# Kernel tuning notes

Hardware: AMD Instinct MI355X
Metric: run time of the kernel (lower is better)

Reference implementation:

```python
import jax, jax.numpy as jnp
import numpy as np

N_NODES = 50000
N_EDGES = 800000
HIDDEN = 256
OUT_DIM = 10
LN_EPS = 1e-5


def setup_inputs() -> dict:
    key = jax.random.key(0)
    ks = jax.random.split(key, 8)
    return {
        "node_features": jax.random.normal(ks[0], (N_NODES, 2), dtype=jnp.float32),
        "edge_index": jax.random.randint(ks[1], (2, N_EDGES), 0, N_NODES, dtype=jnp.int64),
        "W_gcn": jax.random.normal(ks[2], (2, HIDDEN), dtype=jnp.float32) / np.sqrt(2.0),
        "b_gcn": jnp.zeros((HIDDEN,), dtype=jnp.float32),
        "ln_gamma": jnp.ones((HIDDEN,), dtype=jnp.float32),
        "ln_beta": jnp.zeros((HIDDEN,), dtype=jnp.float32),
        "W_h": jax.random.normal(ks[3], (HIDDEN, HIDDEN), dtype=jnp.float32) / np.sqrt(HIDDEN),
        "b_h": jnp.zeros((HIDDEN,), dtype=jnp.float32),
        "W_out": jax.random.normal(ks[4], (HIDDEN, OUT_DIM), dtype=jnp.float32) / np.sqrt(HIDDEN),
        "b_out": jnp.zeros((OUT_DIM,), dtype=jnp.float32),
    }


def reference(node_features, edge_index, W_gcn, b_gcn, ln_gamma, ln_beta, W_h, b_h, W_out, b_out):
    N = node_features.shape[0]
    # --- GCNConv (PyG default): add self-loops + symmetric normalization ---
    loop = jnp.arange(N, dtype=edge_index.dtype)
    src = jnp.concatenate([edge_index[0], loop])
    dst = jnp.concatenate([edge_index[1], loop])
    deg = jax.ops.segment_sum(jnp.ones_like(dst, dtype=node_features.dtype), dst, num_segments=N)
    dinv = jnp.where(deg > 0, jax.lax.rsqrt(deg), 0.0)
    norm = dinv[src] * dinv[dst]  # [E+N]
    h = node_features @ W_gcn  # [N, H], d_in=2 so linear-before-propagate
    msgs = h[src] * norm[:, None]  # [E+N, H] gathered messages
    agg = jax.ops.segment_sum(msgs, dst, num_segments=N) + b_gcn  # scatter-add
    h = jax.nn.relu(agg)
    # --- LayerNorm ---
    mu = jnp.mean(h, axis=-1, keepdims=True)
    var = jnp.mean(jnp.square(h - mu), axis=-1, keepdims=True)
    h = (h - mu) * jax.lax.rsqrt(var + LN_EPS) * ln_gamma + ln_beta
    # --- global_add_pool with batch = zeros(N): one graph ---
    pooled = jnp.sum(h, axis=0, keepdims=True)  # [1, H]
    # --- MLP head ---
    z = jax.nn.relu(pooled @ W_h + b_h)
    logits = z @ W_out + b_out  # [1, OUT_DIM]
    return jax.nn.log_softmax(logits, axis=1)
```

## Files before the change

kernel.cpp:

```cpp
#include <hip/hip_runtime.h>
#include <math.h>

#define N_NODES 50000
#define N_EDGES 800000
#define HIDDEN  256
#define OUT_DIM 10
#define LN_EPS  1e-5f

#define NP    8
#define PART  6250
#define ES    32
#define EPSE  (N_EDGES / ES)
#define EPSE4 (EPSE / 4)
#define NH2   (N_NODES / 2)
#define NPB   64
#define LNB   ((N_NODES + NPB - 1) / NPB)

__global__ __launch_bounds__(1024) void hist_kernel(
    const int4* __restrict__ dst4, unsigned* __restrict__ degp32,
    float* __restrict__ pooled8,
    const float4* __restrict__ Wh4, const float4* __restrict__ Wo4)
{
    __shared__ unsigned hist[PART];
    const int tid = threadIdx.x;
    const int s = blockIdx.x, p = blockIdx.y;
    const int gb = p * ES + s;

    if (gb == 0) { pooled8[tid] = 0.f; pooled8[tid + 1024] = 0.f; }
    if (gb < 17) {
        const int idx = gb * 1024 + tid;
        if (idx < 16384) {
            const float4 v = Wh4[idx];
            asm volatile("" :: "v"(v.x + v.y + v.z + v.w));
        } else if (idx < 17024) {
            const float4 v = Wo4[idx - 16384];
            asm volatile("" :: "v"(v.x + v.y + v.z + v.w));
        }
    }

    for (int i = tid; i < PART; i += 1024) hist[i] = 0u;
    __syncthreads();

    const int base = p * PART;
    const int b0 = s * EPSE4;
    for (int i = tid; i < EPSE4; i += 1024) {
        const int4 d = dst4[b0 + i];
        unsigned r;
        r = (unsigned)(d.x - base); if (r < PART) atomicAdd(&hist[r], 1u);
        r = (unsigned)(d.y - base); if (r < PART) atomicAdd(&hist[r], 1u);
        r = (unsigned)(d.z - base); if (r < PART) atomicAdd(&hist[r], 1u);
        r = (unsigned)(d.w - base); if (r < PART) atomicAdd(&hist[r], 1u);
    }
    __syncthreads();

    unsigned* outp = degp32 + (size_t)s * NH2 + base / 2;
    for (int i = tid; i < PART / 2; i += 1024)
        outp[i] = (hist[2 * i] & 0xFFFFu) | (hist[2 * i + 1] << 16);
}

__global__ __launch_bounds__(256) void dinv_y_kernel(
    const unsigned* __restrict__ degp32, const float4* __restrict__ nf4,
    float2* __restrict__ dinv2, float4* __restrict__ y4)
{
    const int t = blockIdx.x * 256 + threadIdx.x;
    if (t >= NH2) return;
    unsigned s0 = 0, s1 = 0;
    #pragma unroll
    for (int s = 0; s < ES; ++s) {
        const unsigned d = degp32[(size_t)s * NH2 + t];
        s0 += d & 0xFFFFu;
        s1 += d >> 16;
    }
    const float di0 = rsqrtf((float)s0 + 1.0f);
    const float di1 = rsqrtf((float)s1 + 1.0f);
    dinv2[t] = make_float2(di0, di1);
    const float4 x = nf4[t];
    y4[t] = make_float4(di0 * x.x, di0 * x.y, di1 * x.z, di1 * x.w);
}

__global__ __launch_bounds__(1024) void scatterp_kernel(
    const int4* __restrict__ src4, const int4* __restrict__ dst4,
    const float2* __restrict__ y, float2* __restrict__ Tpart2)
{
    __shared__ float Tl[2 * PART];
    const int tid = threadIdx.x;
    const int s = blockIdx.x, p = blockIdx.y;

    for (int i = tid; i < 2 * PART; i += 1024) Tl[i] = 0.f;
    __syncthreads();

    const int base = p * PART;
    const int b0 = s * EPSE4;
    for (int i = tid; i < EPSE4; i += 1024) {
        const int4 d = dst4[b0 + i];
        const int4 sv = src4[b0 + i];
        unsigned r;
        r = (unsigned)(d.x - base);
        if (r < PART) { const float2 ys = y[sv.x]; atomicAdd(&Tl[2*r], ys.x); atomicAdd(&Tl[2*r+1], ys.y); }
        r = (unsigned)(d.y - base);
        if (r < PART) { const float2 ys = y[sv.y]; atomicAdd(&Tl[2*r], ys.x); atomicAdd(&Tl[2*r+1], ys.y); }
        r = (unsigned)(d.z - base);
        if (r < PART) { const float2 ys = y[sv.z]; atomicAdd(&Tl[2*r], ys.x); atomicAdd(&Tl[2*r+1], ys.y); }
        r = (unsigned)(d.w - base);
        if (r < PART) { const float2 ys = y[sv.w]; atomicAdd(&Tl[2*r], ys.x); atomicAdd(&Tl[2*r+1], ys.y); }
    }
    __syncthreads();

    float2* outp = Tpart2 + (size_t)s * N_NODES + base;
    const float2* Tl2 = (const float2*)Tl;
    for (int i = tid; i < PART; i += 1024) outp[i] = Tl2[i];
}

__global__ __launch_bounds__(256) void reduceS_kernel(
    const float2* __restrict__ Tpart2, const float2* __restrict__ y,
    const float* __restrict__ dinv, float2* __restrict__ S2,
    unsigned* __restrict__ mlp_ticket)
{
    const int n = blockIdx.x * 256 + threadIdx.x;
    if (blockIdx.x == 0 && threadIdx.x == 0) *mlp_ticket = 0u;
    if (n >= N_NODES) return;
    float ax = 0.f, ay = 0.f;
    #pragma unroll
    for (int ss = 0; ss < ES; ++ss) {
        const float2 v = Tpart2[(size_t)ss * N_NODES + n];
        ax += v.x; ay += v.y;
    }
    const float di = dinv[n];
    const float2 yn = y[n];
    S2[n] = make_float2(di * (ax + yn.x), di * (ay + yn.y));
}

__global__ __launch_bounds__(256) void ln_pool_mlp_kernel(
    const float2* __restrict__ S2,
    const float* __restrict__ Wg, const float* __restrict__ bg,
    const float* __restrict__ gamma, const float* __restrict__ beta,
    const float* __restrict__ Wh, const float* __restrict__ bh,
    const float* __restrict__ Wo, const float* __restrict__ bo,
    float* __restrict__ pooled8,
    unsigned* __restrict__ ticket,
    float* __restrict__ out)
{
    const int tid  = threadIdx.x;
    const int bid  = blockIdx.x;
    const int n0   = bid * NPB;
    const int lane = tid & 63;
    const int wv   = tid >> 6;

    __shared__ float4 nd[NPB];
    __shared__ float  ps[4][NPB];
    __shared__ float  qs[4][NPB];
    __shared__ float  red[4][HIDDEN];
    __shared__ float  pz[HIDDEN], zz[HIDDEN];
    __shared__ float  lgp[OUT_DIM][16], lg[OUT_DIM];
    __shared__ int    is_last;

    if (tid < NPB) {
        const int n = n0 + tid;
        float2 s = make_float2(0.f, 0.f);
        if (n < N_NODES) s = S2[n];
        nd[tid] = make_float4(s.x, s.y, 0.f, 0.f);
    }
    __syncthreads();

    {
        const int jgu = __builtin_amdgcn_readfirstlane(wv);
        const float* w0p = Wg + jgu * 64;
        const float* w1p = Wg + HIDDEN + jgu * 64;
        const float* bgp = bg + jgu * 64;
        const float4 d = nd[lane];
        float sumA = 0.f, sumB = 0.f, sqA = 0.f, sqB = 0.f;
        #pragma unroll 8
        for (int j = 0; j < 64; j += 2) {
            const float va = fmaxf(fmaf(d.y, w1p[j],     fmaf(d.x, w0p[j],     bgp[j])),     0.f);
            const float vb = fmaxf(fmaf(d.y, w1p[j + 1], fmaf(d.x, w0p[j + 1], bgp[j + 1])), 0.f);
            sumA += va; sqA = fmaf(va, va, sqA);
            sumB += vb; sqB = fmaf(vb, vb, sqB);
        }
        ps[wv][lane] = sumA + sumB;
        qs[wv][lane] = sqA + sqB;
    }
    __syncthreads();

    if (tid < NPB) {
        const float sum = ps[0][tid] + ps[1][tid] + ps[2][tid] + ps[3][tid];
        const float sq  = qs[0][tid] + qs[1][tid] + qs[2][tid] + qs[3][tid];
        const float mu  = sum * (1.0f / HIDDEN);
        const float var = sq * (1.0f / HIDDEN) - mu * mu;
        float r = rsqrtf(var + LN_EPS);
        if (n0 + tid >= N_NODES) r = 0.f;
        const float4 d = nd[tid];
        nd[tid] = make_float4(d.x, d.y, r, r * mu);
    }
    __syncthreads();

    {
        const float4 w0  = *reinterpret_cast<const float4*>(&Wg[lane * 4]);
        const float4 w1  = *reinterpret_cast<const float4*>(&Wg[HIDDEN + lane * 4]);
        const float4 bgv = *reinterpret_cast<const float4*>(&bg[lane * 4]);

        float a0 = 0.f, a1 = 0.f, a2 = 0.f, a3 = 0.f;
        #pragma unroll
        for (int k = 0; k < 16; ++k) {
            const float4 d = nd[wv * 16 + k];
            const float v0 = fmaxf(fmaf(d.y, w1.x, fmaf(d.x, w0.x, bgv.x)), 0.f);
            const float v1 = fmaxf(fmaf(d.y, w1.y, fmaf(d.x, w0.y, bgv.y)), 0.f);
            const float v2 = fmaxf(fmaf(d.y, w1.z, fmaf(d.x, w0.z, bgv.z)), 0.f);
            const float v3 = fmaxf(fmaf(d.y, w1.w, fmaf(d.x, w0.w, bgv.w)), 0.f);
            a0 += fmaf(d.z, v0, -d.w);
            a1 += fmaf(d.z, v1, -d.w);
            a2 += fmaf(d.z, v2, -d.w);
            a3 += fmaf(d.z, v3, -d.w);
        }
        red[wv][lane * 4 + 0] = a0;
        red[wv][lane * 4 + 1] = a1;
        red[wv][lane * 4 + 2] = a2;
        red[wv][lane * 4 + 3] = a3;
    }
    __syncthreads();

    atomicAdd(&pooled8[(bid & 7) * HIDDEN + tid],
              red[0][tid] + red[1][tid] + red[2][tid] + red[3][tid]);
    __syncthreads();

    if (tid == 0) {
        const unsigned old = __hip_atomic_fetch_add(ticket, 1u, __ATOMIC_ACQ_REL,
                                                    __HIP_MEMORY_SCOPE_AGENT);
        is_last = (old == (unsigned)(gridDim.x - 1));
    }
    __syncthreads();
    if (!is_last) return;

    {
        float S = 0.f;
        #pragma unroll
        for (int k = 0; k < 8; ++k) S += pooled8[k * HIDDEN + tid];
        pz[tid] = gamma[tid] * S + (float)N_NODES * beta[tid];
    }
    __syncthreads();

    {
        float acc = bh[tid];
        #pragma unroll 8
        for (int k = 0; k < HIDDEN; ++k) acc = fmaf(pz[k], Wh[k * HIDDEN + tid], acc);
        zz[tid] = fmaxf(acc, 0.f);
    }
    __syncthreads();

    if (tid < OUT_DIM * 16) {
        const int o = tid >> 4, kc = tid & 15;
        float acc = 0.f;
        #pragma unroll
        for (int k = kc * 16; k < kc * 16 + 16; ++k)
            acc = fmaf(zz[k], Wo[k * OUT_DIM + o], acc);
        lgp[o][kc] = acc;
    }
    __syncthreads();
    if (tid < OUT_DIM) {
        float t = bo[tid];
        #pragma unroll
        for (int q = 0; q < 16; ++q) t += lgp[tid][q];
        lg[tid] = t;
    }
    __syncthreads();

    if (tid == 0) {
        float m = lg[0];
        for (int k = 1; k < OUT_DIM; ++k) m = fmaxf(m, lg[k]);
        float sum = 0.f;
        for (int k = 0; k < OUT_DIM; ++k) sum += expf(lg[k] - m);
        const float lse = m + logf(sum);
        for (int k = 0; k < OUT_DIM; ++k) out[k] = lg[k] - lse;
    }
}

extern "C" void kernel_launch(void* const* d_in, const int* in_sizes, int n_in,
                              void* d_out, int out_size, void* d_ws, size_t ws_size,
                              hipStream_t stream) {
    const float* nf    = (const float*)d_in[0];
    const int*   ei    = (const int*)  d_in[1];
    const float* Wg    = (const float*)d_in[2];
    const float* bg    = (const float*)d_in[3];
    const float* gamma = (const float*)d_in[4];
    const float* beta  = (const float*)d_in[5];
    const float* Wh    = (const float*)d_in[6];
    const float* bh    = (const float*)d_in[7];
    const float* Wo    = (const float*)d_in[8];
    const float* bo    = (const float*)d_in[9];
    float* out = (float*)d_out;

    const int* srcp = ei;
    const int* dstp = ei + N_EDGES;

    float* pooled8 = (float*)d_ws;
    unsigned* mlp_ticket = (unsigned*)(pooled8 + 8 * HIDDEN);
    unsigned* degp32 = mlp_ticket + 16;
    float* Tpart = (float*)(degp32 + (size_t)ES * NH2);
    float* dinvp = Tpart + (size_t)ES * 2 * N_NODES;
    float* yp    = dinvp + N_NODES;
    float* Sp    = yp + 2 * N_NODES;

    dim3 pg(ES, NP);
    hist_kernel<<<pg, 1024, 0, stream>>>((const int4*)dstp, degp32, pooled8,
                                         (const float4*)Wh, (const float4*)Wo);
    dinv_y_kernel<<<(NH2 + 255) / 256, 256, 0, stream>>>(degp32, (const float4*)nf,
                                                         (float2*)dinvp, (float4*)yp);
    scatterp_kernel<<<pg, 1024, 0, stream>>>((const int4*)srcp, (const int4*)dstp,
                                             (const float2*)yp, (float2*)Tpart);
    reduceS_kernel<<<(N_NODES + 255) / 256, 256, 0, stream>>>((const float2*)Tpart,
                                                              (const float2*)yp, dinvp,
                                                              (float2*)Sp, mlp_ticket);
    ln_pool_mlp_kernel<<<LNB, 256, 0, stream>>>((const float2*)Sp,
                                                Wg, bg, gamma, beta, Wh, bh, Wo, bo,
                                                pooled8, mlp_ticket, out);
}
```

Baseline: 63.99 us.

## Fuse partial-sum reduction into LN kernel with blocked partial layout, skip src loads

Removes the separate reduceS kernel. scatterp now writes per-slice partial sums in a node-block-major layout, so each LN/pool block can read its 64 nodes' 32 partials contiguously and finish the normalization itself. The ticket reset moves into dinv_y_kernel. The scatter also loads the src indices only when at least one of the four destinations falls in the block's partition. This saves one launch and the S round-trip through memory, at the cost of extra reduction work at the start of the LN kernel.

Result: faster. 60.27 us (-5.8%).

```diff
diff --git a/kernel.cpp b/kernel.cpp
--- a/kernel.cpp
+++ b/kernel.cpp
@@ -60,9 +60,11 @@
 
 __global__ __launch_bounds__(256) void dinv_y_kernel(
     const unsigned* __restrict__ degp32, const float4* __restrict__ nf4,
-    float2* __restrict__ dinv2, float4* __restrict__ y4)
+    float2* __restrict__ dinv2, float4* __restrict__ y4,
+    unsigned* __restrict__ mlp_ticket)
 {
     const int t = blockIdx.x * 256 + threadIdx.x;
+    if (t == 0) *mlp_ticket = 0u;
     if (t >= NH2) return;
     unsigned s0 = 0, s1 = 0;
     #pragma unroll
@@ -80,7 +82,7 @@
 
 __global__ __launch_bounds__(1024) void scatterp_kernel(
     const int4* __restrict__ src4, const int4* __restrict__ dst4,
-    const float2* __restrict__ y, float2* __restrict__ Tpart2)
+    const float2* __restrict__ y, float2* __restrict__ TpartB2)
 {
     __shared__ float Tl[2 * PART];
     const int tid = threadIdx.x;
@@ -93,45 +95,32 @@
     const int b0 = s * EPSE4;
     for (int i = tid; i < EPSE4; i += 1024) {
         const int4 d = dst4[b0 + i];
-        const int4 sv = src4[b0 + i];
-        unsigned r;
-        r = (unsigned)(d.x - base);
-        if (r < PART) { const float2 ys = y[sv.x]; atomicAdd(&Tl[2*r], ys.x); atomicAdd(&Tl[2*r+1], ys.y); }
-        r = (unsigned)(d.y - base);
-        if (r < PART) { const float2 ys = y[sv.y]; atomicAdd(&Tl[2*r], ys.x); atomicAdd(&Tl[2*r+1], ys.y); }
-        r = (unsigned)(d.z - base);
-        if (r < PART) { const float2 ys = y[sv.z]; atomicAdd(&Tl[2*r], ys.x); atomicAdd(&Tl[2*r+1], ys.y); }
-        r = (unsigned)(d.w - base);
-        if (r < PART) { const float2 ys = y[sv.w]; atomicAdd(&Tl[2*r], ys.x); atomicAdd(&Tl[2*r+1], ys.y); }
-    }
-    __syncthreads();
-
-    float2* outp = Tpart2 + (size_t)s * N_NODES + base;
+        const unsigned r0 = (unsigned)(d.x - base);
+        const unsigned r1 = (unsigned)(d.y - base);
+        const unsigned r2 = (unsigned)(d.z - base);
+        const unsigned r3 = (unsigned)(d.w - base);
+        if ((r0 < PART) | (r1 < PART) | (r2 < PART) | (r3 < PART)) {
+            const int4 sv = src4[b0 + i];
+            if (r0 < PART) { const float2 ys = y[sv.x]; atomicAdd(&Tl[2*r0], ys.x); atomicAdd(&Tl[2*r0+1], ys.y); }
+            if (r1 < PART) { const float2 ys = y[sv.y]; atomicAdd(&Tl[2*r1], ys.x); atomicAdd(&Tl[2*r1+1], ys.y); }
+            if (r2 < PART) { const float2 ys = y[sv.z]; atomicAdd(&Tl[2*r2], ys.x); atomicAdd(&Tl[2*r2+1], ys.y); }
+            if (r3 < PART) { const float2 ys = y[sv.w]; atomicAdd(&Tl[2*r3], ys.x); atomicAdd(&Tl[2*r3+1], ys.y); }
+        }
+    }
+    __syncthreads();
+
     const float2* Tl2 = (const float2*)Tl;
-    for (int i = tid; i < PART; i += 1024) outp[i] = Tl2[i];
-}
-
-__global__ __launch_bounds__(256) void reduceS_kernel(
-    const float2* __restrict__ Tpart2, const float2* __restrict__ y,
-    const float* __restrict__ dinv, float2* __restrict__ S2,
-    unsigned* __restrict__ mlp_ticket)
-{
-    const int n = blockIdx.x * 256 + threadIdx.x;
-    if (blockIdx.x == 0 && threadIdx.x == 0) *mlp_ticket = 0u;
-    if (n >= N_NODES) return;
-    float ax = 0.f, ay = 0.f;
-    #pragma unroll
-    for (int ss = 0; ss < ES; ++ss) {
-        const float2 v = Tpart2[(size_t)ss * N_NODES + n];
-        ax += v.x; ay += v.y;
-    }
-    const float di = dinv[n];
-    const float2 yn = y[n];
-    S2[n] = make_float2(di * (ax + yn.x), di * (ay + yn.y));
+    for (int i = tid; i < PART; i += 1024) {
+        const int n = base + i;
+        const int idx = (((n >> 6) * ES + s) << 6) | (n & 63);
+        TpartB2[idx] = Tl2[i];
+    }
 }
 
 __global__ __launch_bounds__(256) void ln_pool_mlp_kernel(
-    const float2* __restrict__ S2,
+    const float2* __restrict__ TpartB2,
+    const float2* __restrict__ y,
+    const float* __restrict__ dinv,
     const float* __restrict__ Wg, const float* __restrict__ bg,
     const float* __restrict__ gamma, const float* __restrict__ beta,
     const float* __restrict__ Wh, const float* __restrict__ bh,
@@ -154,11 +143,31 @@
     __shared__ float  lgp[OUT_DIM][16], lg[OUT_DIM];
     __shared__ int    is_last;
 
+    {
+        const float2* tp = TpartB2 + (size_t)bid * (ES * NPB);
+        float ax = 0.f, ay = 0.f;
+        #pragma unroll
+        for (int s8 = 0; s8 < 8; ++s8) {
+            const float2 v = tp[((wv << 3) + s8) * NPB + lane];
+            ax += v.x; ay += v.y;
+        }
+        ps[wv][lane] = ax;
+        qs[wv][lane] = ay;
+    }
+    __syncthreads();
+
     if (tid < NPB) {
         const int n = n0 + tid;
-        float2 s = make_float2(0.f, 0.f);
-        if (n < N_NODES) s = S2[n];
-        nd[tid] = make_float4(s.x, s.y, 0.f, 0.f);
+        float s0 = 0.f, s1 = 0.f;
+        if (n < N_NODES) {
+            const float tx = ps[0][tid] + ps[1][tid] + ps[2][tid] + ps[3][tid];
+            const float ty = qs[0][tid] + qs[1][tid] + qs[2][tid] + qs[3][tid];
+            const float di = dinv[n];
+            const float2 yn = y[n];
+            s0 = di * (tx + yn.x);
+            s1 = di * (ty + yn.y);
+        }
+        nd[tid] = make_float4(s0, s1, 0.f, 0.f);
     }
     __syncthreads();
 
@@ -294,22 +303,20 @@
     float* pooled8 = (float*)d_ws;
     unsigned* mlp_ticket = (unsigned*)(pooled8 + 8 * HIDDEN);
     unsigned* degp32 = mlp_ticket + 16;
-    float* Tpart = (float*)(degp32 + (size_t)ES * NH2);
-    float* dinvp = Tpart + (size_t)ES * 2 * N_NODES;
-    float* yp    = dinvp + N_NODES;
-    float* Sp    = yp + 2 * N_NODES;
+    float* TpartB = (float*)(degp32 + (size_t)ES * NH2);
+    float* dinvp  = TpartB + (size_t)LNB * ES * NPB * 2;
+    float* yp     = dinvp + N_NODES;
 
     dim3 pg(ES, NP);
     hist_kernel<<<pg, 1024, 0, stream>>>((const int4*)dstp, degp32, pooled8,
                                          (const float4*)Wh, (const float4*)Wo);
     dinv_y_kernel<<<(NH2 + 255) / 256, 256, 0, stream>>>(degp32, (const float4*)nf,
-                                                         (float2*)dinvp, (float4*)yp);
+                                                         (float2*)dinvp, (float4*)yp,
+                                                         mlp_ticket);
     scatterp_kernel<<<pg, 1024, 0, stream>>>((const int4*)srcp, (const int4*)dstp,
-                                             (const float2*)yp, (float2*)Tpart);
-    reduceS_kernel<<<(N_NODES + 255) / 256, 256, 0, stream>>>((const float2*)Tpart,
-                                                              (const float2*)yp, dinvp,
-                                                              (float2*)Sp, mlp_ticket);
-    ln_pool_mlp_kernel<<<LNB, 256, 0, stream>>>((const float2*)Sp,
+                                             (const float2*)yp, (float2*)TpartB);
+    ln_pool_mlp_kernel<<<LNB, 256, 0, stream>>>((const float2*)TpartB,
+                                                (const float2*)yp, dinvp,
                                                 Wg, bg, gamma, beta, Wh, bh, Wo, bo,
                                                 pooled8, mlp_ticket, out);
 }
```
